# Performance work log

Measured on AMD Instinct MI355X. Metric: run time of the kernel, lower is better.

The kernel has to match this reference:

```python
import jax, jax.numpy as jnp
import numpy as np

NHEAD = 8
NPTS = 4

def _bilinear_sample(E_flat, locs, H, W):
    # E_flat: [B, H*W, D] channel-last flattened feature map
    # locs:   [B, N, 2] normalized (x, y) in [-1, 1], align_corners=False, zeros padding
    ix = ((locs[..., 0] + 1.0) * W - 1.0) * 0.5
    iy = ((locs[..., 1] + 1.0) * H - 1.0) * 0.5
    x0 = jnp.floor(ix); y0 = jnp.floor(iy)
    x1 = x0 + 1.0;      y1 = y0 + 1.0
    wx1 = ix - x0; wx0 = 1.0 - wx1
    wy1 = iy - y0; wy0 = 1.0 - wy1
    gather = jax.vmap(lambda e, i: e[i])  # per-batch gather -> [B, N, D]
    def corner(xc, yc, w):
        valid = (xc >= 0) & (xc < W) & (yc >= 0) & (yc < H)
        xi = jnp.clip(xc, 0, W - 1).astype(jnp.int32)
        yi = jnp.clip(yc, 0, H - 1).astype(jnp.int32)
        g = gather(E_flat, yi * W + xi)
        return g * (w * valid)[..., None]
    return (corner(x0, y0, wx0 * wy0) + corner(x1, y0, wx1 * wy0)
            + corner(x0, y1, wx0 * wy1) + corner(x1, y1, wx1 * wy1))

def setup_inputs() -> dict:
    key = jax.random.key(0)
    ks = jax.random.split(key, 6)
    B, M, D = 8, 1024, 256
    H, Wd = 100, 100
    SADQ = jax.random.normal(ks[0], (B, M, D), jnp.float32)
    E = jax.random.normal(ks[1], (B, H * Wd, D), jnp.float32)
    # learned params (random instead of the degenerate zero-init, so the math is exercised)
    Wo = jax.random.normal(ks[2], (D, NHEAD * NPTS * 2), jnp.float32) * 0.02
    bo = jnp.zeros((NHEAD * NPTS * 2,), jnp.float32)
    Wa = jax.random.normal(ks[3], (D, NHEAD * NPTS), jnp.float32) * 0.05
    ba = jnp.zeros((NHEAD * NPTS,), jnp.float32)
    Wr = jax.random.normal(ks[4], (D, 2), jnp.float32) * 0.05
    br = jnp.zeros((2,), jnp.float32)
    Wp = jax.random.normal(ks[5], (D, D), jnp.float32) * 0.05
    bp = jnp.zeros((D,), jnp.float32)
    return {"SADQ": SADQ, "E": E, "Wo": Wo, "bo": bo, "Wa": Wa, "ba": ba,
            "Wr": Wr, "br": br, "Wp": Wp, "bp": bp, "H": H, "W": Wd}

def reference(SADQ, E, Wo, bo, Wa, ba, Wr, br, Wp, bp, H, W):
    B, M, D = SADQ.shape
    offsets = (SADQ @ Wo + bo).reshape(B, M, NHEAD, NPTS, 2)
    attn = jax.nn.softmax((SADQ @ Wa + ba).reshape(B, M, NHEAD, NPTS), axis=-1)
    base_ref = (SADQ @ Wr + br)[:, :, None, None, :]            # [B, M, 1, 1, 2]
    locs = (base_ref + offsets * 0.1).reshape(B, M * NHEAD * NPTS, 2)
    sampled = _bilinear_sample(E, locs, H, W).reshape(B, M, NHEAD, NPTS, D)
    # sum over points, mean over heads, fused into one contraction
    agg = jnp.einsum('bmhpd,bmhp->bmd', sampled, attn) / NHEAD
    return agg @ Wp + bp
```

## Files before the change

### kernel.cpp

```cpp
#include <hip/hip_runtime.h>
#include <hip/hip_bf16.h>
#include <math.h>

#define BATCH 8
#define MQ    1024
#define DIM   256
#define NHEAD 8
#define NPTS  4
#define NPROJ 98
#define PSTR  112

typedef __attribute__((ext_vector_type(8))) short  short8;
typedef __attribute__((ext_vector_type(4))) float  f32x4;

static __device__ __forceinline__ ushort f2bf(float f) {
    union { float f; unsigned u; } v; v.f = f;
    const unsigned r = v.u + 0x7fffu + ((v.u >> 16) & 1u);
    return (ushort)(r >> 16);
}

#define KEEP4(v) asm volatile("" : "+v"(v.x), "+v"(v.y), "+v"(v.z), "+v"(v.w))

__global__ __launch_bounds__(112) void wcat_build_kernel(
    const float* __restrict__ Wo, const float* __restrict__ bo,
    const float* __restrict__ Wa, const float* __restrict__ ba,
    const float* __restrict__ Wr, const float* __restrict__ br,
    float* __restrict__ Wcat, float* __restrict__ bcat)
{
    const int k = blockIdx.x;
    const int j = threadIdx.x;
    float w = 0.f, bias = 0.f;
    if (j < 64)      { w = Wo[k * 64 + j];        bias = bo[j]; }
    else if (j < 96) { w = Wa[k * 32 + (j - 64)]; bias = ba[j - 64]; }
    else if (j < 98) { w = Wr[k * 2  + (j - 96)]; bias = br[j - 96]; }
    Wcat[k * PSTR + j] = w;
    if (k == 0) bcat[j] = bias;
}

__global__ __launch_bounds__(256) void proj_kernel(
    const float* __restrict__ SADQ,
    const float* __restrict__ Wcat,
    const float* __restrict__ bcat,
    float* __restrict__ P)
{
    __shared__ float Qs[16][36];
    __shared__ float Ws[32][112];

    const int tid  = threadIdx.x;
    const int row0 = blockIdx.x * 16;
    const int rg   = tid >> 4;
    const int cg   = tid & 15;

    float acc[7] = {};

    for (int kc = 0; kc < DIM; kc += 32) {
        if (tid < 128) {
            const int r  = tid >> 3;
            const int k4 = (tid & 7) * 4;
            const float4 v = *(const float4*)&SADQ[(size_t)(row0 + r) * DIM + kc + k4];
            Qs[r][k4 + 0] = v.x; Qs[r][k4 + 1] = v.y;
            Qs[r][k4 + 2] = v.z; Qs[r][k4 + 3] = v.w;
        }
        for (int fi = tid; fi < 32 * 28; fi += 256) {
            const int k  = fi / 28;
            const int j4 = (fi % 28) * 4;
            *(float4*)&Ws[k][j4] = *(const float4*)&Wcat[(size_t)(kc + k) * PSTR + j4];
        }
        __syncthreads();

        #pragma unroll 8
        for (int k = 0; k < 32; ++k) {
            const float q = Qs[rg][k];
            #pragma unroll
            for (int j = 0; j < 7; ++j)
                acc[j] = fmaf(q, Ws[k][cg * 7 + j], acc[j]);
        }
        __syncthreads();
    }

    #pragma unroll
    for (int j = 0; j < 7; ++j) {
        const int col = cg * 7 + j;
        P[(size_t)(row0 + rg) * PSTR + col] = acc[j] + bcat[col];
    }
}

__global__ __launch_bounds__(256) void gather_kernel(
    const float* __restrict__ P,
    const float* __restrict__ E,
    const int*   __restrict__ Hp, const int* __restrict__ Wdp,
    ushort* __restrict__ aggb)
{
    const int tid  = threadIdx.x;
    const int wid  = tid >> 6;
    const int lane = tid & 63;
    const int bid  = blockIdx.x;
    const int cpx  = (int)(gridDim.x >> 3);
    const int sb   = (bid & 7) * cpx + (bid >> 3);
    const int row  = sb * 4 + wid;
    const int b    = row >> 10;

    __shared__ float sW[4][128];
    __shared__ int   sIdx[4][128];

    const int Hh = *Hp;
    const int Ww = *Wdp;

    if (lane < 32) {
        const int p = lane;
        const float* Pr = P + (size_t)row * PSTR;
        const float lg = Pr[64 + p];
        float mx = fmaxf(lg, __shfl_xor(lg, 1));
        mx = fmaxf(mx, __shfl_xor(mx, 2));
        const float e = expf(lg - mx);
        float s = e + __shfl_xor(e, 1);
        s += __shfl_xor(s, 2);
        const float aw = e / s * (1.f / NHEAD);

        const float lx = Pr[96] + 0.1f * Pr[p * 2 + 0];
        const float ly = Pr[97] + 0.1f * Pr[p * 2 + 1];
        const float ix = ((lx + 1.f) * (float)Ww - 1.f) * 0.5f;
        const float iy = ((ly + 1.f) * (float)Hh - 1.f) * 0.5f;
        const float x0f = floorf(ix), y0f = floorf(iy);
        const int   x0  = (int)x0f,   y0  = (int)y0f;
        const float wx1 = ix - x0f, wx0 = 1.f - wx1;
        const float wy1 = iy - y0f, wy0 = 1.f - wy1;

        #pragma unroll
        for (int c = 0; c < 4; ++c) {
            const int   xc = x0 + (c & 1);
            const int   yc = y0 + (c >> 1);
            const float wx = (c & 1) ? wx1 : wx0;
            const float wy = (c >> 1) ? wy1 : wy0;
            const bool valid = (xc >= 0) && (xc < Ww) && (yc >= 0) && (yc < Hh);
            const int xi = min(max(xc, 0), Ww - 1);
            const int yi = min(max(yc, 0), Hh - 1);
            sW  [wid][p * 4 + c] = valid ? (wx * wy * aw) : 0.f;
            sIdx[wid][p * 4 + c] = (yi * Ww + xi) * (DIM / 4);
        }
    }
    __syncthreads();

    const float4* __restrict__ Eb4 =
        (const float4*)(E + (size_t)b * (size_t)(Hh * Ww) * DIM);

    float4 acc = make_float4(0.f, 0.f, 0.f, 0.f);
    for (int t = 0; t < 128; t += 8) {
        const float w0 = sW[wid][t + 0]; const int i0 = sIdx[wid][t + 0];
        const float w1 = sW[wid][t + 1]; const int i1 = sIdx[wid][t + 1];
        const float w2 = sW[wid][t + 2]; const int i2 = sIdx[wid][t + 2];
        const float w3 = sW[wid][t + 3]; const int i3 = sIdx[wid][t + 3];
        const float w4 = sW[wid][t + 4]; const int i4 = sIdx[wid][t + 4];
        const float w5 = sW[wid][t + 5]; const int i5 = sIdx[wid][t + 5];
        const float w6 = sW[wid][t + 6]; const int i6 = sIdx[wid][t + 6];
        const float w7 = sW[wid][t + 7]; const int i7 = sIdx[wid][t + 7];

        float4 e0 = Eb4[(size_t)i0 + lane];
        float4 e1 = Eb4[(size_t)i1 + lane];
        float4 e2 = Eb4[(size_t)i2 + lane];
        float4 e3 = Eb4[(size_t)i3 + lane];
        float4 e4 = Eb4[(size_t)i4 + lane];
        float4 e5 = Eb4[(size_t)i5 + lane];
        float4 e6 = Eb4[(size_t)i6 + lane];
        float4 e7 = Eb4[(size_t)i7 + lane];
        KEEP4(e0); KEEP4(e1); KEEP4(e2); KEEP4(e3);
        KEEP4(e4); KEEP4(e5); KEEP4(e6); KEEP4(e7);

        acc.x = fmaf(w0, e0.x, acc.x); acc.y = fmaf(w0, e0.y, acc.y);
        acc.z = fmaf(w0, e0.z, acc.z); acc.w = fmaf(w0, e0.w, acc.w);
        acc.x = fmaf(w1, e1.x, acc.x); acc.y = fmaf(w1, e1.y, acc.y);
        acc.z = fmaf(w1, e1.z, acc.z); acc.w = fmaf(w1, e1.w, acc.w);
        acc.x = fmaf(w2, e2.x, acc.x); acc.y = fmaf(w2, e2.y, acc.y);
        acc.z = fmaf(w2, e2.z, acc.z); acc.w = fmaf(w2, e2.w, acc.w);
        acc.x = fmaf(w3, e3.x, acc.x); acc.y = fmaf(w3, e3.y, acc.y);
        acc.z = fmaf(w3, e3.z, acc.z); acc.w = fmaf(w3, e3.w, acc.w);
        acc.x = fmaf(w4, e4.x, acc.x); acc.y = fmaf(w4, e4.y, acc.y);
        acc.z = fmaf(w4, e4.z, acc.z); acc.w = fmaf(w4, e4.w, acc.w);
        acc.x = fmaf(w5, e5.x, acc.x); acc.y = fmaf(w5, e5.y, acc.y);
        acc.z = fmaf(w5, e5.z, acc.z); acc.w = fmaf(w5, e5.w, acc.w);
        acc.x = fmaf(w6, e6.x, acc.x); acc.y = fmaf(w6, e6.y, acc.y);
        acc.z = fmaf(w6, e6.z, acc.z); acc.w = fmaf(w6, e6.w, acc.w);
        acc.x = fmaf(w7, e7.x, acc.x); acc.y = fmaf(w7, e7.y, acc.y);
        acc.z = fmaf(w7, e7.z, acc.z); acc.w = fmaf(w7, e7.w, acc.w);
    }

    ushort4 o;
    o.x = f2bf(acc.x); o.y = f2bf(acc.y);
    o.z = f2bf(acc.z); o.w = f2bf(acc.w);
    *(ushort4*)&aggb[(size_t)row * DIM + lane * 4] = o;
}

__global__ __launch_bounds__(256) void wp_convert_kernel(
    const float* __restrict__ Wp, ushort* __restrict__ WpT)
{
    const int k = blockIdx.x;
    const int n = threadIdx.x;
    WpT[(size_t)n * DIM + k] = f2bf(Wp[(size_t)k * DIM + n]);
}

__global__ __launch_bounds__(256) void mfma_gemm_kernel(
    const ushort* __restrict__ A,
    const ushort* __restrict__ BT,
    const float*  __restrict__ bp,
    float* __restrict__ out)
{
    __shared__ ushort ldsA[64 * 40];
    __shared__ ushort ldsB[64 * 40];

    const int tid  = threadIdx.x;
    const int mb   = blockIdx.x * 64;
    const int nb   = blockIdx.y * 64;
    const int wave = tid >> 6;
    const int lane = tid & 63;
    const int r0   = (wave >> 1) * 32;
    const int c0   = (wave & 1) * 32;
    const int lrow = lane & 15;
    const int kgrp = lane >> 4;

    const int sm = tid >> 2;
    const int sc = (tid & 3) * 8;

    f32x4 acc00 = {0.f, 0.f, 0.f, 0.f};
    f32x4 acc01 = {0.f, 0.f, 0.f, 0.f};
    f32x4 acc10 = {0.f, 0.f, 0.f, 0.f};
    f32x4 acc11 = {0.f, 0.f, 0.f, 0.f};

    for (int kb = 0; kb < DIM; kb += 32) {
        *(uint4*)&ldsA[sm * 40 + sc] =
            *(const uint4*)&A[(size_t)(mb + sm) * DIM + kb + sc];
        *(uint4*)&ldsB[sm * 40 + sc] =
            *(const uint4*)&BT[(size_t)(nb + sm) * DIM + kb + sc];
        __syncthreads();

        const short8 a0 = *(const short8*)&ldsA[(r0 + lrow)      * 40 + kgrp * 8];
        const short8 a1 = *(const short8*)&ldsA[(r0 + 16 + lrow) * 40 + kgrp * 8];
        const short8 b0 = *(const short8*)&ldsB[(c0 + lrow)      * 40 + kgrp * 8];
        const short8 b1 = *(const short8*)&ldsB[(c0 + 16 + lrow) * 40 + kgrp * 8];

        acc00 = __builtin_amdgcn_mfma_f32_16x16x32_bf16(a0, b0, acc00, 0, 0, 0);
        acc01 = __builtin_amdgcn_mfma_f32_16x16x32_bf16(a0, b1, acc01, 0, 0, 0);
        acc10 = __builtin_amdgcn_mfma_f32_16x16x32_bf16(a1, b0, acc10, 0, 0, 0);
        acc11 = __builtin_amdgcn_mfma_f32_16x16x32_bf16(a1, b1, acc11, 0, 0, 0);
        __syncthreads();
    }

    const int orow = mb + r0 + kgrp * 4;
    const int ocol = nb + c0 + lrow;
    const float bp0 = bp[ocol];
    const float bp1 = bp[ocol + 16];
    #pragma unroll
    for (int reg = 0; reg < 4; ++reg) {
        out[(size_t)(orow + reg)      * DIM + ocol]      = acc00[reg] + bp0;
        out[(size_t)(orow + reg)      * DIM + ocol + 16] = acc01[reg] + bp1;
        out[(size_t)(orow + 16 + reg) * DIM + ocol]      = acc10[reg] + bp0;
        out[(size_t)(orow + 16 + reg) * DIM + ocol + 16] = acc11[reg] + bp1;
    }
}

extern "C" void kernel_launch(void* const* d_in, const int* in_sizes, int n_in,
                              void* d_out, int out_size, void* d_ws, size_t ws_size,
                              hipStream_t stream)
{
    const float* SADQ = (const float*)d_in[0];
    const float* E    = (const float*)d_in[1];
    const float* Wo   = (const float*)d_in[2];
    const float* bo   = (const float*)d_in[3];
    const float* Wa   = (const float*)d_in[4];
    const float* ba   = (const float*)d_in[5];
    const float* Wr   = (const float*)d_in[6];
    const float* br   = (const float*)d_in[7];
    const float* Wp   = (const float*)d_in[8];
    const float* bp   = (const float*)d_in[9];
    const int*   Hp   = (const int*)d_in[10];
    const int*   Wdp  = (const int*)d_in[11];

    const int BM = in_sizes[0] / DIM;

    char* ws = (char*)d_ws;
    ushort* aggb = (ushort*)(ws);
    ushort* WpT  = (ushort*)(ws + 4194304);
    float*  P    = (float*) (ws + 4194304 + 131072);
    float*  Wcat = (float*) (ws + 4194304 + 131072 + 3670016);
    float*  bcat = (float*) (ws + 4194304 + 131072 + 3670016 + 114688);
    float*  out  = (float*)d_out;

    wcat_build_kernel<<<DIM, PSTR, 0, stream>>>(Wo, bo, Wa, ba, Wr, br, Wcat, bcat);
    proj_kernel<<<BM / 16, 256, 0, stream>>>(SADQ, Wcat, bcat, P);
    gather_kernel<<<BM / 4, 256, 0, stream>>>(P, E, Hp, Wdp, aggb);
    wp_convert_kernel<<<DIM, 256, 0, stream>>>(Wp, WpT);

    dim3 g2(BM / 64, DIM / 64);
    mfma_gemm_kernel<<<g2, 256, 0, stream>>>(aggb, WpT, bp, out);
}
```

Baseline: 226.2 us.

## Run projection GEMM on bf16 MFMA with hi/lo split for fp32 accuracy

Replaces the scalar fp32 FMA projection kernel with an MFMA bf16 GEMM. SADQ and the concatenated projection weights are each split into bf16 high and low parts, and three MFMA products (hh, hl, lh) recover near-fp32 precision. This adds a separate split pass over SADQ and extra workspace traffic in exchange for using matrix cores on the projection.

Result: faster. 204.1 us (-9.8%).

```diff
diff --git a/kernel.cpp b/kernel.cpp
--- a/kernel.cpp
+++ b/kernel.cpp
@@ -9,6 +9,7 @@
 #define NPTS  4
 #define NPROJ 98
 #define PSTR  112
+#define NPAD  128
 
 typedef __attribute__((ext_vector_type(8))) short  short8;
 typedef __attribute__((ext_vector_type(4))) float  f32x4;
@@ -18,70 +19,129 @@
     const unsigned r = v.u + 0x7fffu + ((v.u >> 16) & 1u);
     return (ushort)(r >> 16);
 }
+static __device__ __forceinline__ float bf2f(ushort h) {
+    union { unsigned u; float f; } v; v.u = ((unsigned)h) << 16;
+    return v.f;
+}
 
 #define KEEP4(v) asm volatile("" : "+v"(v.x), "+v"(v.y), "+v"(v.z), "+v"(v.w))
 
-__global__ __launch_bounds__(112) void wcat_build_kernel(
+__global__ __launch_bounds__(256) void sadq_split_kernel(
+    const float* __restrict__ SADQ, ushort* __restrict__ Ahi,
+    ushort* __restrict__ Alo)
+{
+    const size_t i4 = (size_t)blockIdx.x * 256 + threadIdx.x;
+    const float4 v = ((const float4*)SADQ)[i4];
+    ushort4 hi, lo;
+    hi.x = f2bf(v.x); lo.x = f2bf(v.x - bf2f(hi.x));
+    hi.y = f2bf(v.y); lo.y = f2bf(v.y - bf2f(hi.y));
+    hi.z = f2bf(v.z); lo.z = f2bf(v.z - bf2f(hi.z));
+    hi.w = f2bf(v.w); lo.w = f2bf(v.w - bf2f(hi.w));
+    ((ushort4*)Ahi)[i4] = hi;
+    ((ushort4*)Alo)[i4] = lo;
+}
+
+__global__ __launch_bounds__(128) void wsplit_build_kernel(
     const float* __restrict__ Wo, const float* __restrict__ bo,
     const float* __restrict__ Wa, const float* __restrict__ ba,
     const float* __restrict__ Wr, const float* __restrict__ br,
-    float* __restrict__ Wcat, float* __restrict__ bcat)
+    ushort* __restrict__ WcTh, ushort* __restrict__ WcTl,
+    float* __restrict__ bcat)
 {
     const int k = blockIdx.x;
-    const int j = threadIdx.x;
+    const int n = threadIdx.x;
     float w = 0.f, bias = 0.f;
-    if (j < 64)      { w = Wo[k * 64 + j];        bias = bo[j]; }
-    else if (j < 96) { w = Wa[k * 32 + (j - 64)]; bias = ba[j - 64]; }
-    else if (j < 98) { w = Wr[k * 2  + (j - 96)]; bias = br[j - 96]; }
-    Wcat[k * PSTR + j] = w;
-    if (k == 0) bcat[j] = bias;
-}
-
-__global__ __launch_bounds__(256) void proj_kernel(
-    const float* __restrict__ SADQ,
-    const float* __restrict__ Wcat,
-    const float* __restrict__ bcat,
+    if (n < 64)      { w = Wo[k * 64 + n];        bias = bo[n]; }
+    else if (n < 96) { w = Wa[k * 32 + (n - 64)]; bias = ba[n - 64]; }
+    else if (n < 98) { w = Wr[k * 2  + (n - 96)]; bias = br[n - 96]; }
+    const ushort hi = f2bf(w);
+    const ushort lo = f2bf(w - bf2f(hi));
+    WcTh[(size_t)n * DIM + k] = hi;
+    WcTl[(size_t)n * DIM + k] = lo;
+    if (k == 0) bcat[n] = bias;
+}
+
+__global__ __launch_bounds__(256) void proj_mfma_kernel(
+    const ushort* __restrict__ Ahi,
+    const ushort* __restrict__ Alo,
+    const ushort* __restrict__ BTh,
+    const ushort* __restrict__ BTl,
+    const float*  __restrict__ bcat,
     float* __restrict__ P)
 {
-    __shared__ float Qs[16][36];
-    __shared__ float Ws[32][112];
+    __shared__ ushort ldsAh[64 * 40];
+    __shared__ ushort ldsAl[64 * 40];
+    __shared__ ushort ldsBh[64 * 40];
+    __shared__ ushort ldsBl[64 * 40];
 
     const int tid  = threadIdx.x;
-    const int row0 = blockIdx.x * 16;
-    const int rg   = tid >> 4;
-    const int cg   = tid & 15;
-
-    float acc[7] = {};
-
-    for (int kc = 0; kc < DIM; kc += 32) {
-        if (tid < 128) {
-            const int r  = tid >> 3;
-            const int k4 = (tid & 7) * 4;
-            const float4 v = *(const float4*)&SADQ[(size_t)(row0 + r) * DIM + kc + k4];
-            Qs[r][k4 + 0] = v.x; Qs[r][k4 + 1] = v.y;
-            Qs[r][k4 + 2] = v.z; Qs[r][k4 + 3] = v.w;
+    const int mb   = blockIdx.x * 64;
+    const int nb   = blockIdx.y * 64;
+    const int wave = tid >> 6;
+    const int lane = tid & 63;
+    const int r0   = (wave >> 1) * 32;
+    const int c0   = (wave & 1) * 32;
+    const int lrow = lane & 15;
+    const int kgrp = lane >> 4;
+
+    const int sm = tid >> 2;
+    const int sc = (tid & 3) * 8;
+
+    f32x4 acc00 = {0.f, 0.f, 0.f, 0.f};
+    f32x4 acc01 = {0.f, 0.f, 0.f, 0.f};
+    f32x4 acc10 = {0.f, 0.f, 0.f, 0.f};
+    f32x4 acc11 = {0.f, 0.f, 0.f, 0.f};
+
+    for (int kb = 0; kb < DIM; kb += 32) {
+        *(uint4*)&ldsAh[sm * 40 + sc] =
+            *(const uint4*)&Ahi[(size_t)(mb + sm) * DIM + kb + sc];
+        *(uint4*)&ldsAl[sm * 40 + sc] =
+            *(const uint4*)&Alo[(size_t)(mb + sm) * DIM + kb + sc];
+        *(uint4*)&ldsBh[sm * 40 + sc] =
+            *(const uint4*)&BTh[(size_t)(nb + sm) * DIM + kb + sc];
+        *(uint4*)&ldsBl[sm * 40 + sc] =
+            *(const uint4*)&BTl[(size_t)(nb + sm) * DIM + kb + sc];
+        __syncthreads();
+
+        const short8 a0h = *(const short8*)&ldsAh[(r0 + lrow)      * 40 + kgrp * 8];
+        const short8 a1h = *(const short8*)&ldsAh[(r0 + 16 + lrow) * 40 + kgrp * 8];
+        const short8 a0l = *(const short8*)&ldsAl[(r0 + lrow)      * 40 + kgrp * 8];
+        const short8 a1l = *(const short8*)&ldsAl[(r0 + 16 + lrow) * 40 + kgrp * 8];
+        const short8 b0h = *(const short8*)&ldsBh[(c0 + lrow)      * 40 + kgrp * 8];
+        const short8 b1h = *(const short8*)&ldsBh[(c0 + 16 + lrow) * 40 + kgrp * 8];
+        const short8 b0l = *(const short8*)&ldsBl[(c0 + lrow)      * 40 + kgrp * 8];
+        const short8 b1l = *(const short8*)&ldsBl[(c0 + 16 + lrow) * 40 + kgrp * 8];
+
+        acc00 = __builtin_amdgcn_mfma_f32_16x16x32_bf16(a0h, b0h, acc00, 0, 0, 0);
+        acc01 = __builtin_amdgcn_mfma_f32_16x16x32_bf16(a0h, b1h, acc01, 0, 0, 0);
+        acc10 = __builtin_amdgcn_mfma_f32_16x16x32_bf16(a1h, b0h, acc10, 0, 0, 0);
+        acc11 = __builtin_amdgcn_mfma_f32_16x16x32_bf16(a1h, b1h, acc11, 0, 0, 0);
+        acc00 = __builtin_amdgcn_mfma_f32_16x16x32_bf16(a0h, b0l, acc00, 0, 0, 0);
+        acc01 = __builtin_amdgcn_mfma_f32_16x16x32_bf16(a0h, b1l, acc01, 0, 0, 0);
+        acc10 = __builtin_amdgcn_mfma_f32_16x16x32_bf16(a1h, b0l, acc10, 0, 0, 0);
+        acc11 = __builtin_amdgcn_mfma_f32_16x16x32_bf16(a1h, b1l, acc11, 0, 0, 0);
+        acc00 = __builtin_amdgcn_mfma_f32_16x16x32_bf16(a0l, b0h, acc00, 0, 0, 0);
+        acc01 = __builtin_amdgcn_mfma_f32_16x16x32_bf16(a0l, b1h, acc01, 0, 0, 0);
+        acc10 = __builtin_amdgcn_mfma_f32_16x16x32_bf16(a1l, b0h, acc10, 0, 0, 0);
+        acc11 = __builtin_amdgcn_mfma_f32_16x16x32_bf16(a1l, b1h, acc11, 0, 0, 0);
+        __syncthreads();
+    }
+
+    const int orow  = mb + r0 + kgrp * 4;
+    const int ocol0 = nb + c0 + lrow;
+    const int ocol1 = ocol0 + 16;
+    const float bc0 = bcat[ocol0];
+    const float bc1 = bcat[ocol1];
+    #pragma unroll
+    for (int reg = 0; reg < 4; ++reg) {
+        if (ocol0 < PSTR) {
+            P[(size_t)(orow + reg)      * PSTR + ocol0] = acc00[reg] + bc0;
+            P[(size_t)(orow + 16 + reg) * PSTR + ocol0] = acc10[reg] + bc0;
         }
-        for (int fi = tid; fi < 32 * 28; fi += 256) {
-            const int k  = fi / 28;
-            const int j4 = (fi % 28) * 4;
-            *(float4*)&Ws[k][j4] = *(const float4*)&Wcat[(size_t)(kc + k) * PSTR + j4];
+        if (ocol1 < PSTR) {
+            P[(size_t)(orow + reg)      * PSTR + ocol1] = acc01[reg] + bc1;
+            P[(size_t)(orow + 16 + reg) * PSTR + ocol1] = acc11[reg] + bc1;
         }
-        __syncthreads();
-
-        #pragma unroll 8
-        for (int k = 0; k < 32; ++k) {
-            const float q = Qs[rg][k];
-            #pragma unroll
-            for (int j = 0; j < 7; ++j)
-                acc[j] = fmaf(q, Ws[k][cg * 7 + j], acc[j]);
-        }
-        __syncthreads();
-    }
-
-    #pragma unroll
-    for (int j = 0; j < 7; ++j) {
-        const int col = cg * 7 + j;
-        P[(size_t)(row0 + rg) * PSTR + col] = acc[j] + bcat[col];
     }
 }
 
@@ -279,13 +339,20 @@
     char* ws = (char*)d_ws;
     ushort* aggb = (ushort*)(ws);
     ushort* WpT  = (ushort*)(ws + 4194304);
-    float*  P    = (float*) (ws + 4194304 + 131072);
-    float*  Wcat = (float*) (ws + 4194304 + 131072 + 3670016);
-    float*  bcat = (float*) (ws + 4194304 + 131072 + 3670016 + 114688);
+    float*  P    = (float*) (ws + 4325376);
+    ushort* WcTh = (ushort*)(ws + 7995392);
+    ushort* WcTl = (ushort*)(ws + 8060928);
+    float*  bcat = (float*) (ws + 8126464);
+    ushort* Ahi  = (ushort*)(ws + 8126976);
+    ushort* Alo  = (ushort*)(ws + 12321280);
     float*  out  = (float*)d_out;
 
-    wcat_build_kernel<<<DIM, PSTR, 0, stream>>>(Wo, bo, Wa, ba, Wr, br, Wcat, bcat);
-    proj_kernel<<<BM / 16, 256, 0, stream>>>(SADQ, Wcat, bcat, P);
+    sadq_split_kernel<<<(BM * DIM / 4) / 256, 256, 0, stream>>>(SADQ, Ahi, Alo);
+    wsplit_build_kernel<<<DIM, NPAD, 0, stream>>>(Wo, bo, Wa, ba, Wr, br,
+                                                  WcTh, WcTl, bcat);
+    dim3 gp(BM / 64, NPAD / 64);
+    proj_mfma_kernel<<<gp, 256, 0, stream>>>(Ahi, Alo, WcTh, WcTl, bcat, P);
+
     gather_kernel<<<BM / 4, 256, 0, stream>>>(P, E, Hp, Wdp, aggb);
     wp_convert_kernel<<<DIM, 256, 0, stream>>>(Wp, WpT);
 
```
